# Optimization experiments

Hardware: AMD Instinct MI355X
Metric: run time of the kernel (lower is better)

## Reference

```python
import jax, jax.numpy as jnp
import numpy as np

C = 512        # num_channels
HEADS = 8      # num_channels // num_head_channels
DH = 64        # num_head_channels
G = 32         # num_groups
EPS = 1e-5
SCALE = DH ** -0.25  # pre-multiplied into q and k (scale applied twice -> 1/sqrt(DH))


def setup_inputs() -> dict:
    key = jax.random.key(0)
    ks = jax.random.split(key, 10)
    B, H, W = 2, 64, 64
    def w(k):
        return jax.random.normal(k, (C, C), jnp.float32) * 0.02
    def b(k):
        return jax.random.normal(k, (C,), jnp.float32) * 0.02
    return {
        "x": jax.random.normal(ks[0], (B, C, H, W), jnp.float32),
        "gn_w": jnp.ones((C,), jnp.float32),
        "gn_b": jnp.zeros((C,), jnp.float32),
        "wq": w(ks[1]), "bq": b(ks[2]),
        "wk": w(ks[3]), "bk": b(ks[4]),
        "wv": w(ks[5]), "bv": b(ks[6]),
        "wp": w(ks[7]), "bp": b(ks[8]),
    }


def reference(x, gn_w, gn_b, wq, bq, wk, bk, wv, bv, wp, bp):
    B, Cc, H, W = x.shape
    # GroupNorm over (C/G, H, W) per group
    xr = x.reshape(B, G, Cc // G, H * W)
    mean = xr.mean(axis=(2, 3), keepdims=True)
    var = xr.var(axis=(2, 3), keepdims=True)
    h = ((xr - mean) * jax.lax.rsqrt(var + EPS)).reshape(B, Cc, H, W)
    h = h * gn_w[None, :, None, None] + gn_b[None, :, None, None]
    # B C H W -> B (H W) C
    t = h.reshape(B, Cc, H * W).transpose(0, 2, 1)
    # q/k pre-multiplied by SCALE (equivalent to pre_multiply_weights_by_scale)
    q = (t @ wq.T + bq) * SCALE
    k = (t @ wk.T + bk) * SCALE
    v = t @ wv.T + bv
    def split_heads(a):  # B HW (h d) -> B h HW d
        return a.reshape(B, H * W, HEADS, DH).transpose(0, 2, 1, 3)
    q, k, v = split_heads(q), split_heads(k), split_heads(v)
    # full HWxHW score matrix, softmax over keys
    attn = jax.nn.softmax(jnp.einsum('bhqd,bhkd->bhqk', q, k), axis=-1)
    o = jnp.einsum('bhqk,bhkd->bhqd', attn, v)
    o = o.transpose(0, 2, 1, 3).reshape(B, H * W, Cc)  # join heads
    o = o @ wp.T + bp
    # B (H W) C -> B C H W, residual
    return o.transpose(0, 2, 1).reshape(B, Cc, H, W) + x
```

## Files before the change

kernel.cpp:

```cpp
#include <hip/hip_runtime.h>

#define HWN 4096
#define CCH 512
#define NHEAD 8
#define DHD 64
#define NBATCH 2
#define QK_SCALE 0.35355339059327373f
#define LOG2E    1.4426950408889634f

using floatx4 = __attribute__((ext_vector_type(4))) float;
using bf16x8  = __attribute__((ext_vector_type(8))) short;
using bf16x4  = __attribute__((ext_vector_type(4))) short;

__device__ __forceinline__ unsigned short f2b(float f) {
  union { float f; unsigned u; } x; x.f = f;
  unsigned r = x.u + 0x7FFFu + ((x.u >> 16) & 1u);
  return (unsigned short)(r >> 16);
}

__device__ __forceinline__ float fast_exp2(float x) {
#if __has_builtin(__builtin_amdgcn_exp2f)
  return __builtin_amdgcn_exp2f(x);
#else
  return __expf(x * 0.69314718056f);
#endif
}

__device__ __forceinline__ unsigned pack_bf16_trunc(float lo, float hi) {
  return __builtin_amdgcn_perm(__float_as_uint(hi), __float_as_uint(lo), 0x07060302u);
}

__global__ __launch_bounds__(256) void gn_stats(const float* __restrict__ x,
                                                float* __restrict__ stat) {
  int bg = blockIdx.x;
  const float4* p = (const float4*)(x + (size_t)bg * 65536) + blockIdx.y * 2048;
  float s = 0.f, ss = 0.f;
  for (int i = threadIdx.x; i < 2048; i += 256) {
    float4 v = p[i];
    s  += v.x + v.y + v.z + v.w;
    ss += v.x*v.x + v.y*v.y + v.z*v.z + v.w*v.w;
  }
  for (int off = 32; off; off >>= 1) {
    s  += __shfl_xor(s, off);
    ss += __shfl_xor(ss, off);
  }
  __shared__ float red[8];
  int w = threadIdx.x >> 6;
  if ((threadIdx.x & 63) == 0) { red[w] = s; red[4 + w] = ss; }
  __syncthreads();
  if (threadIdx.x == 0) {
    float S  = red[0] + red[1] + red[2] + red[3];
    float SS = red[4] + red[5] + red[6] + red[7];
    atomicAdd(&stat[bg], S);
    atomicAdd(&stat[64 + bg], SS);
  }
}

__global__ __launch_bounds__(256) void prep_w(
    const float* __restrict__ wq, const float* __restrict__ wk,
    const float* __restrict__ wv, const float* __restrict__ wp,
    const float* __restrict__ bq, const float* __restrict__ bk,
    const float* __restrict__ bv,
    unsigned short* __restrict__ Wqkv, unsigned short* __restrict__ Wp,
    float* __restrict__ bqkv) {
  int i = blockIdx.x * 256 + threadIdx.x;
  if (i < 786432) {
    int row = i >> 9;
    float v;
    if (row < 512)       v = wq[i] * (QK_SCALE * LOG2E);
    else if (row < 1024) v = wk[i - 262144] * QK_SCALE;
    else                 v = wv[i - 524288];
    Wqkv[i] = f2b(v);
  } else if (i < 1048576) {
    Wp[i - 786432] = f2b(wp[i - 786432]);
  } else if (i < 1050112) {
    int j = i - 1048576;
    float v = (j < 512) ? bq[j] * (QK_SCALE * LOG2E)
            : (j < 1024) ? bk[j - 512] * QK_SCALE
            : bv[j - 1024];
    bqkv[j] = v;
  }
}

__global__ __launch_bounds__(256) void gn_apply(
    const float* __restrict__ x, const float* __restrict__ stat,
    const float* __restrict__ gnw, const float* __restrict__ gnb,
    unsigned short* __restrict__ t) {
  int pt = blockIdx.x & 63;
  int ct = (blockIdx.x >> 6) & 7;
  int b  = blockIdx.x >> 9;
  int c0 = ct * 64, p0 = pt * 64;
  __shared__ float tile[64][68];
  int tid = threadIdx.x;
  for (int pp = 0; pp < 4; ++pp) {
    int f = (pp * 256 + tid) * 4;
    int cl = f >> 6, pl = f & 63;
    int c = c0 + cl;
    float4 v = *(const float4*)(x + ((size_t)(b * 512 + c)) * 4096 + p0 + pl);
    int g = c >> 4;
    float S    = stat[b * 32 + g];
    float SS   = stat[64 + b * 32 + g];
    float mean = S * (1.f / 65536.f);
    float var  = SS * (1.f / 65536.f) - mean * mean;
    float rstd = rsqrtf(var + 1e-5f);
    float w  = gnw[c] * rstd;
    float bb = gnb[c] - mean * w;
    tile[cl][pl + 0] = v.x * w + bb;
    tile[cl][pl + 1] = v.y * w + bb;
    tile[cl][pl + 2] = v.z * w + bb;
    tile[cl][pl + 3] = v.w * w + bb;
  }
  __syncthreads();
  for (int pp = 0; pp < 2; ++pp) {
    int f = (pp * 256 + tid) * 8;
    int pl = f >> 6, cl = f & 63;
    unsigned short u[8];
#pragma unroll
    for (int j = 0; j < 8; ++j) u[j] = f2b(tile[cl + j][pl]);
    *(uint4*)(t + ((size_t)(b * 4096 + p0 + pl)) * 512 + c0 + cl) = *(uint4*)u;
  }
}

__global__ __launch_bounds__(256) void gemm_qkv(
    const unsigned short* __restrict__ t, const unsigned short* __restrict__ Wqkv,
    const float* __restrict__ bqkv,
    unsigned short* __restrict__ qo, unsigned short* __restrict__ ko,
    unsigned short* __restrict__ vo) {
  int M0 = blockIdx.x * 64;
  int N0 = blockIdx.y * 64;
  __shared__ unsigned short At[64][72];
  __shared__ unsigned short Bt[64][72];
  int tid = threadIdx.x, w = tid >> 6, l = tid & 63;
  int quad = l >> 4, m16 = l & 15;
  floatx4 acc[4] = {};
  for (int k0 = 0; k0 < 512; k0 += 64) {
    __syncthreads();
#pragma unroll
    for (int pp = 0; pp < 2; ++pp) {
      int f = (pp * 256 + tid) * 8;
      int r = f >> 6, c = f & 63;
      *(uint4*)&At[r][c] = *(const uint4*)(t    + (size_t)(M0 + r) * 512 + k0 + c);
      *(uint4*)&Bt[r][c] = *(const uint4*)(Wqkv + (size_t)(N0 + r) * 512 + k0 + c);
    }
    __syncthreads();
    bf16x8 af0 = *(const bf16x8*)&At[w * 16 + m16][quad * 8];
    bf16x8 af1 = *(const bf16x8*)&At[w * 16 + m16][32 + quad * 8];
#pragma unroll
    for (int nt = 0; nt < 4; ++nt) {
      bf16x8 b0 = *(const bf16x8*)&Bt[nt * 16 + m16][quad * 8];
      bf16x8 b1 = *(const bf16x8*)&Bt[nt * 16 + m16][32 + quad * 8];
      acc[nt] = __builtin_amdgcn_mfma_f32_16x16x32_bf16(af0, b0, acc[nt], 0, 0, 0);
      acc[nt] = __builtin_amdgcn_mfma_f32_16x16x32_bf16(af1, b1, acc[nt], 0, 0, 0);
    }
  }
  int which = N0 >> 9;
  int head  = (N0 & 511) >> 6;
  if (which == 2) {
    __syncthreads();
#pragma unroll
    for (int nt = 0; nt < 4; ++nt) {
      int d = nt * 16 + m16;
      float bias = bqkv[N0 + d];
#pragma unroll
      for (int r = 0; r < 4; ++r)
        At[d][w * 16 + quad * 4 + r] = f2b(acc[nt][r] + bias);
    }
    __syncthreads();
    int bb = M0 >> 12, p0 = M0 & 4095;
    unsigned short* dst = vo + ((size_t)(bb * 8 + head) * 64) * 4096;
#pragma unroll
    for (int pp = 0; pp < 2; ++pp) {
      int f = (pp * 256 + tid) * 8;
      int d = f >> 6, pl = f & 63;
      *(uint4*)(dst + (size_t)d * 4096 + p0 + pl) = *(uint4*)&At[d][pl];
    }
  } else {
    unsigned short* dst = (which == 0) ? qo : ko;
#pragma unroll
    for (int nt = 0; nt < 4; ++nt) {
      int n = N0 + nt * 16 + m16;
      float bias = bqkv[n];
      int d = n & 63;
#pragma unroll
      for (int r = 0; r < 4; ++r) {
        int m = M0 + w * 16 + quad * 4 + r;
        int b = m >> 12, p = m & 4095;
        dst[(((size_t)(b * 8 + head) * 4096 + p) << 6) + d] = f2b(acc[nt][r] + bias);
      }
    }
  }
}

__global__ __launch_bounds__(256, 2) void attn(
    const unsigned short* __restrict__ q, const unsigned short* __restrict__ k,
    const unsigned short* __restrict__ vt, unsigned short* __restrict__ o) {
  int qt = blockIdx.x;
  int bh = blockIdx.y;
  int b = bh >> 3, h = bh & 7;
  __shared__ unsigned short Kt[128][72];
  __shared__ unsigned short Vt[64][136];
  int tid = threadIdx.x, w = tid >> 6, l = tid & 63;
  int quad = l >> 4, m16 = l & 15;
  const size_t base = (size_t)bh * HWN * DHD;
  int krow_base = ((m16 >> 2) * 8) + (m16 & 3);

  bf16x8 qfA0, qfA1, qfB0, qfB1;
  {
    int qrow = qt * 128 + w * 32 + m16;
    const unsigned short* qp = q + base + (size_t)qrow * 64 + quad * 8;
    qfA0 = *(const bf16x8*)qp;
    qfA1 = *(const bf16x8*)(qp + 32);
    qfB0 = *(const bf16x8*)(qp + 16 * 64);
    qfB1 = *(const bf16x8*)(qp + 16 * 64 + 32);
  }
  bf16x8 ones;
#pragma unroll
  for (int z = 0; z < 8; ++z) ones[z] = (short)0x3F80;

  floatx4 accOA[4] = {}, accOB[4] = {};
  floatx4 accLA = {}, accLB = {};
  float mrowA = -1e30f, mrowB = -1e30f;

  for (int kt = 0; kt < 32; ++kt) {
    __syncthreads();
#pragma unroll
    for (int pp = 0; pp < 4; ++pp) {
      int f = (pp * 256 + tid) * 8;
      int rk = f >> 6, ck = f & 63;
      *(uint4*)&Kt[rk][ck] = *(const uint4*)(k + base + (size_t)(kt * 128 + rk) * 64 + ck);
      int rv = f >> 7, cv = f & 127;
      *(uint4*)&Vt[rv][cv] = *(const uint4*)(vt + base + (size_t)rv * 4096 + kt * 128 + cv);
    }
    __syncthreads();
    floatx4 sA[8], sB[8];
#pragma unroll
    for (int nt = 0; nt < 4; ++nt)
#pragma unroll
      for (int hh = 0; hh < 2; ++hh) {
        int row = nt * 32 + hh * 4 + krow_base;
        bf16x8 kf0 = *(const bf16x8*)&Kt[row][quad * 8];
        bf16x8 kf1 = *(const bf16x8*)&Kt[row][32 + quad * 8];
        floatx4 zA = {}, zB = {};
        zA = __builtin_amdgcn_mfma_f32_16x16x32_bf16(kf0, qfA0, zA, 0, 0, 0);
        sA[nt * 2 + hh] = __builtin_amdgcn_mfma_f32_16x16x32_bf16(kf1, qfA1, zA, 0, 0, 0);
        zB = __builtin_amdgcn_mfma_f32_16x16x32_bf16(kf0, qfB0, zB, 0, 0, 0);
        sB[nt * 2 + hh] = __builtin_amdgcn_mfma_f32_16x16x32_bf16(kf1, qfB1, zB, 0, 0, 0);
      }
    float mxA = sA[0][0], mxB = sB[0][0];
#pragma unroll
    for (int nt = 0; nt < 8; ++nt)
#pragma unroll
      for (int i = 0; i < 4; ++i) {
        mxA = fmaxf(mxA, sA[nt][i]);
        mxB = fmaxf(mxB, sB[nt][i]);
      }
    mxA = fmaxf(mxA, __shfl_xor(mxA, 16));
    mxA = fmaxf(mxA, __shfl_xor(mxA, 32));
    mxB = fmaxf(mxB, __shfl_xor(mxB, 16));
    mxB = fmaxf(mxB, __shfl_xor(mxB, 32));
    bool grew = (mxA > mrowA) || (mxB > mrowB);
    float mnA = fmaxf(mrowA, mxA);
    float mnB = fmaxf(mrowB, mxB);
#pragma unroll
    for (int nt = 0; nt < 8; ++nt)
#pragma unroll
      for (int i = 0; i < 4; ++i) {
        sA[nt][i] = fast_exp2(sA[nt][i] - mnA);
        sB[nt][i] = fast_exp2(sB[nt][i] - mnB);
      }
    if (__ballot(grew)) {
      float aA = fast_exp2(mrowA - mnA);
      float aB = fast_exp2(mrowB - mnB);
      float a0 = __shfl(aA, quad * 4 + 0), b0 = __shfl(aB, quad * 4 + 0);
      float a1 = __shfl(aA, quad * 4 + 1), b1 = __shfl(aB, quad * 4 + 1);
      float a2 = __shfl(aA, quad * 4 + 2), b2 = __shfl(aB, quad * 4 + 2);
      float a3 = __shfl(aA, quad * 4 + 3), b3 = __shfl(aB, quad * 4 + 3);
#pragma unroll
      for (int dt = 0; dt < 4; ++dt) {
        accOA[dt][0] *= a0; accOA[dt][1] *= a1; accOA[dt][2] *= a2; accOA[dt][3] *= a3;
        accOB[dt][0] *= b0; accOB[dt][1] *= b1; accOB[dt][2] *= b2; accOB[dt][3] *= b3;
      }
      accLA[0] *= a0; accLA[1] *= a1; accLA[2] *= a2; accLA[3] *= a3;
      accLB[0] *= b0; accLB[1] *= b1; accLB[2] *= b2; accLB[3] *= b3;
    }
    mrowA = mnA; mrowB = mnB;
    bf16x8 pfA[4], pfB[4];
#pragma unroll
    for (int nt = 0; nt < 4; ++nt) {
      union { unsigned u[4]; bf16x8 v; } pa, pb;
      pa.u[0] = pack_bf16_trunc(sA[nt * 2][0],     sA[nt * 2][1]);
      pa.u[1] = pack_bf16_trunc(sA[nt * 2][2],     sA[nt * 2][3]);
      pa.u[2] = pack_bf16_trunc(sA[nt * 2 + 1][0], sA[nt * 2 + 1][1]);
      pa.u[3] = pack_bf16_trunc(sA[nt * 2 + 1][2], sA[nt * 2 + 1][3]);
      pfA[nt] = pa.v;
      pb.u[0] = pack_bf16_trunc(sB[nt * 2][0],     sB[nt * 2][1]);
      pb.u[1] = pack_bf16_trunc(sB[nt * 2][2],     sB[nt * 2][3]);
      pb.u[2] = pack_bf16_trunc(sB[nt * 2 + 1][0], sB[nt * 2 + 1][1]);
      pb.u[3] = pack_bf16_trunc(sB[nt * 2 + 1][2], sB[nt * 2 + 1][3]);
      pfB[nt] = pb.v;
    }
#pragma unroll
    for (int dt = 0; dt < 4; ++dt) {
#pragma unroll
      for (int nt = 0; nt < 4; ++nt) {
        bf16x8 vf = *(const bf16x8*)&Vt[dt * 16 + m16][nt * 32 + quad * 8];
        accOA[dt] = __builtin_amdgcn_mfma_f32_16x16x32_bf16(pfA[nt], vf, accOA[dt], 0, 0, 0);
        accOB[dt] = __builtin_amdgcn_mfma_f32_16x16x32_bf16(pfB[nt], vf, accOB[dt], 0, 0, 0);
      }
    }
#pragma unroll
    for (int nt = 0; nt < 4; ++nt) {
      accLA = __builtin_amdgcn_mfma_f32_16x16x32_bf16(pfA[nt], ones, accLA, 0, 0, 0);
      accLB = __builtin_amdgcn_mfma_f32_16x16x32_bf16(pfB[nt], ones, accLB, 0, 0, 0);
    }
  }
  float lA0 = 1.f / accLA[0], lA1 = 1.f / accLA[1], lA2 = 1.f / accLA[2], lA3 = 1.f / accLA[3];
  float lB0 = 1.f / accLB[0], lB1 = 1.f / accLB[1], lB2 = 1.f / accLB[2], lB3 = 1.f / accLB[3];
#pragma unroll
  for (int dt = 0; dt < 4; ++dt) {
    int d = dt * 16 + m16;
    int qrowA = qt * 128 + w * 32 + quad * 4;
    size_t rowb = ((size_t)(b * 4096 + qrowA)) * 512 + h * 64 + d;
    o[rowb]           = f2b(accOA[dt][0] * lA0);
    o[rowb + 512]     = f2b(accOA[dt][1] * lA1);
    o[rowb + 1024]    = f2b(accOA[dt][2] * lA2);
    o[rowb + 1536]    = f2b(accOA[dt][3] * lA3);
    size_t rowb2 = rowb + (size_t)16 * 512;
    o[rowb2]          = f2b(accOB[dt][0] * lB0);
    o[rowb2 + 512]    = f2b(accOB[dt][1] * lB1);
    o[rowb2 + 1024]   = f2b(accOB[dt][2] * lB2);
    o[rowb2 + 1536]   = f2b(accOB[dt][3] * lB3);
  }
}

__global__ __launch_bounds__(256) void gemm_out(
    const unsigned short* __restrict__ o, const unsigned short* __restrict__ Wp,
    const float* __restrict__ bp, const float* __restrict__ x,
    float* __restrict__ out) {
  int C0 = blockIdx.x * 64, P0 = blockIdx.y * 64, b = blockIdx.z;
  __shared__ unsigned short At[64][72];
  __shared__ unsigned short Bt[64][72];
  int tid = threadIdx.x, w = tid >> 6, l = tid & 63;
  int quad = l >> 4, m16 = l & 15;
  floatx4 acc[4] = {};
  for (int k0 = 0; k0 < 512; k0 += 64) {
    __syncthreads();
#pragma unroll
    for (int pp = 0; pp < 2; ++pp) {
      int f = (pp * 256 + tid) * 8;
      int r = f >> 6, c = f & 63;
      *(uint4*)&At[r][c] = *(const uint4*)(Wp + (size_t)(C0 + r) * 512 + k0 + c);
      *(uint4*)&Bt[r][c] = *(const uint4*)(o + ((size_t)(b * 4096 + P0 + r)) * 512 + k0 + c);
    }
    __syncthreads();
    bf16x8 af0 = *(const bf16x8*)&At[w * 16 + m16][quad * 8];
    bf16x8 af1 = *(const bf16x8*)&At[w * 16 + m16][32 + quad * 8];
#pragma unroll
    for (int nt = 0; nt < 4; ++nt) {
      bf16x8 b0 = *(const bf16x8*)&Bt[nt * 16 + m16][quad * 8];
      bf16x8 b1 = *(const bf16x8*)&Bt[nt * 16 + m16][32 + quad * 8];
      acc[nt] = __builtin_amdgcn_mfma_f32_16x16x32_bf16(af0, b0, acc[nt], 0, 0, 0);
      acc[nt] = __builtin_amdgcn_mfma_f32_16x16x32_bf16(af1, b1, acc[nt], 0, 0, 0);
    }
  }
#pragma unroll
  for (int r = 0; r < 4; ++r) {
    int c = C0 + w * 16 + quad * 4 + r;
    float bias = bp[c];
#pragma unroll
    for (int nt = 0; nt < 4; ++nt) {
      int p = P0 + nt * 16 + m16;
      size_t idx = ((size_t)(b * 512 + c)) * 4096 + p;
      out[idx] = acc[nt][r] + bias + x[idx];
    }
  }
}

extern "C" void kernel_launch(void* const* d_in, const int* in_sizes, int n_in,
                              void* d_out, int out_size, void* d_ws, size_t ws_size,
                              hipStream_t stream) {
  const float* x   = (const float*)d_in[0];
  const float* gnw = (const float*)d_in[1];
  const float* gnb = (const float*)d_in[2];
  const float* wq  = (const float*)d_in[3];
  const float* bq  = (const float*)d_in[4];
  const float* wk  = (const float*)d_in[5];
  const float* bk  = (const float*)d_in[6];
  const float* wv  = (const float*)d_in[7];
  const float* bv  = (const float*)d_in[8];
  const float* wp  = (const float*)d_in[9];
  const float* bp  = (const float*)d_in[10];
  float* out = (float*)d_out;

  char* ws = (char*)d_ws;
  float* stat          = (float*)ws;          ws += 1024;
  float* bqkv          = (float*)ws;          ws += 8192;
  unsigned short* Wqkv = (unsigned short*)ws; ws += (size_t)1536 * 512 * 2;
  unsigned short* Wp   = (unsigned short*)ws; ws += (size_t)512 * 512 * 2;
  unsigned short* t    = (unsigned short*)ws; ws += (size_t)8192 * 512 * 2;
  unsigned short* qb   = (unsigned short*)ws; ws += (size_t)8192 * 512 * 2;
  unsigned short* kb   = (unsigned short*)ws; ws += (size_t)8192 * 512 * 2;
  unsigned short* vb   = (unsigned short*)ws; ws += (size_t)8192 * 512 * 2;
  unsigned short* ob   = (unsigned short*)ws; ws += (size_t)8192 * 512 * 2;

  hipMemsetAsync(stat, 0, 512, stream);
  dim3 g0(64, 8);
  gn_stats<<<g0, 256, 0, stream>>>(x, stat);
  prep_w<<<4103, 256, 0, stream>>>(wq, wk, wv, wp, bq, bk, bv, Wqkv, Wp, bqkv);
  gn_apply<<<1024, 256, 0, stream>>>(x, stat, gnw, gnb, t);
  dim3 g1(128, 24);
  gemm_qkv<<<g1, 256, 0, stream>>>(t, Wqkv, bqkv, qb, kb, vb);
  dim3 g2(32, 16);
  attn<<<g2, 256, 0, stream>>>(qb, kb, vb, ob);
  dim3 g3(8, 64, 2);
  gemm_out<<<g3, 256, 0, stream>>>(ob, Wp, bp, x, out);
}
```

Before: 276.2 us.

## Split attention over two key halves and merge partial softmax results

The attention kernel now splits the key range into two halves along a new grid dimension, doubling the block count from 512 to 1024. It also raises the launch-bounds occupancy hint from 2 to 4 blocks. Each block writes a normalized partial output plus its row max and sum, reusing the output buffer and the t buffer as scratch. A new merge kernel rescales and combines the two partials into the final bf16 head output. This targets under-filled CUs (512 blocks on a 256-CU GPU) at the cost of an extra kernel launch, extra memory traffic, and an additional bf16 rounding of the partial outputs.

```diff
diff --git a/kernel.cpp b/kernel.cpp
--- a/kernel.cpp
+++ b/kernel.cpp
@@ -16,6 +16,11 @@
   union { float f; unsigned u; } x; x.f = f;
   unsigned r = x.u + 0x7FFFu + ((x.u >> 16) & 1u);
   return (unsigned short)(r >> 16);
+}
+
+__device__ __forceinline__ float b2f(unsigned short u) {
+  union { unsigned u; float f; } x; x.u = ((unsigned)u) << 16;
+  return x.f;
 }
 
 __device__ __forceinline__ float fast_exp2(float x) {
@@ -191,17 +196,19 @@
   }
 }
 
-__global__ __launch_bounds__(256, 2) void attn(
+__global__ __launch_bounds__(256, 4) void attn(
     const unsigned short* __restrict__ q, const unsigned short* __restrict__ k,
-    const unsigned short* __restrict__ vt, unsigned short* __restrict__ o) {
+    const unsigned short* __restrict__ vt,
+    unsigned short* __restrict__ pO, float* __restrict__ mlbuf) {
   int qt = blockIdx.x;
   int bh = blockIdx.y;
-  int b = bh >> 3, h = bh & 7;
+  int ks = blockIdx.z;
   __shared__ unsigned short Kt[128][72];
   __shared__ unsigned short Vt[64][136];
   int tid = threadIdx.x, w = tid >> 6, l = tid & 63;
   int quad = l >> 4, m16 = l & 15;
   const size_t base = (size_t)bh * HWN * DHD;
+  const int key0 = ks * 2048;
   int krow_base = ((m16 >> 2) * 8) + (m16 & 3);
 
   bf16x8 qfA0, qfA1, qfB0, qfB1;
@@ -221,15 +228,15 @@
   floatx4 accLA = {}, accLB = {};
   float mrowA = -1e30f, mrowB = -1e30f;
 
-  for (int kt = 0; kt < 32; ++kt) {
+  for (int kt = 0; kt < 16; ++kt) {
     __syncthreads();
 #pragma unroll
     for (int pp = 0; pp < 4; ++pp) {
       int f = (pp * 256 + tid) * 8;
       int rk = f >> 6, ck = f & 63;
-      *(uint4*)&Kt[rk][ck] = *(const uint4*)(k + base + (size_t)(kt * 128 + rk) * 64 + ck);
+      *(uint4*)&Kt[rk][ck] = *(const uint4*)(k + base + (size_t)(key0 + kt * 128 + rk) * 64 + ck);
       int rv = f >> 7, cv = f & 127;
-      *(uint4*)&Vt[rv][cv] = *(const uint4*)(vt + base + (size_t)rv * 4096 + kt * 128 + cv);
+      *(uint4*)&Vt[rv][cv] = *(const uint4*)(vt + base + (size_t)rv * 4096 + key0 + kt * 128 + cv);
     }
     __syncthreads();
     floatx4 sA[8], sB[8];
@@ -314,23 +321,70 @@
       accLB = __builtin_amdgcn_mfma_f32_16x16x32_bf16(pfB[nt], ones, accLB, 0, 0, 0);
     }
   }
+  const size_t prow = (size_t)(ks * 16 + bh) * 4096;
   float lA0 = 1.f / accLA[0], lA1 = 1.f / accLA[1], lA2 = 1.f / accLA[2], lA3 = 1.f / accLA[3];
   float lB0 = 1.f / accLB[0], lB1 = 1.f / accLB[1], lB2 = 1.f / accLB[2], lB3 = 1.f / accLB[3];
 #pragma unroll
   for (int dt = 0; dt < 4; ++dt) {
     int d = dt * 16 + m16;
     int qrowA = qt * 128 + w * 32 + quad * 4;
-    size_t rowb = ((size_t)(b * 4096 + qrowA)) * 512 + h * 64 + d;
-    o[rowb]           = f2b(accOA[dt][0] * lA0);
-    o[rowb + 512]     = f2b(accOA[dt][1] * lA1);
-    o[rowb + 1024]    = f2b(accOA[dt][2] * lA2);
-    o[rowb + 1536]    = f2b(accOA[dt][3] * lA3);
-    size_t rowb2 = rowb + (size_t)16 * 512;
-    o[rowb2]          = f2b(accOB[dt][0] * lB0);
-    o[rowb2 + 512]    = f2b(accOB[dt][1] * lB1);
-    o[rowb2 + 1024]   = f2b(accOB[dt][2] * lB2);
-    o[rowb2 + 1536]   = f2b(accOB[dt][3] * lB3);
-  }
+    size_t rb = (prow + qrowA) * 64 + d;
+    pO[rb]        = f2b(accOA[dt][0] * lA0);
+    pO[rb + 64]   = f2b(accOA[dt][1] * lA1);
+    pO[rb + 128]  = f2b(accOA[dt][2] * lA2);
+    pO[rb + 192]  = f2b(accOA[dt][3] * lA3);
+    size_t rb2 = rb + 16 * 64;
+    pO[rb2]       = f2b(accOB[dt][0] * lB0);
+    pO[rb2 + 64]  = f2b(accOB[dt][1] * lB1);
+    pO[rb2 + 128] = f2b(accOB[dt][2] * lB2);
+    pO[rb2 + 192] = f2b(accOB[dt][3] * lB3);
+  }
+  if (m16 < 4) {
+    float mvA = __shfl(mrowA, quad * 4 + m16);
+    float mvB = __shfl(mrowB, quad * 4 + m16);
+    float lvA = (m16 == 0) ? accLA[0] : (m16 == 1) ? accLA[1] : (m16 == 2) ? accLA[2] : accLA[3];
+    float lvB = (m16 == 0) ? accLB[0] : (m16 == 1) ? accLB[1] : (m16 == 2) ? accLB[2] : accLB[3];
+    int qrow = qt * 128 + w * 32 + quad * 4 + m16;
+    float2* mlp = (float2*)mlbuf;
+    float2 va; va.x = mvA; va.y = lvA;
+    float2 vb; vb.x = mvB; vb.y = lvB;
+    mlp[prow + qrow]      = va;
+    mlp[prow + qrow + 16] = vb;
+  }
+}
+
+__global__ __launch_bounds__(256) void attn_merge(
+    const unsigned short* __restrict__ pO, const float* __restrict__ mlbuf,
+    unsigned short* __restrict__ ob) {
+  int r = blockIdx.x * 64 + (threadIdx.x >> 2);
+  int dseg = (threadIdx.x & 3) * 16;
+  int bh = r >> 12, qq = r & 4095;
+  int b = bh >> 3, h = bh & 7;
+  const float2* mlp = (const float2*)mlbuf;
+  float2 ml0 = mlp[r];
+  float2 ml1 = mlp[65536 + r];
+  float ms = fmaxf(ml0.x, ml1.x);
+  float s0 = fast_exp2(ml0.x - ms) * ml0.y;
+  float s1 = fast_exp2(ml1.x - ms) * ml1.y;
+  float inv = 1.f / (s0 + s1);
+  float w0 = s0 * inv, w1 = s1 * inv;
+  const unsigned short* p0 = pO + ((size_t)r * 64 + dseg);
+  const unsigned short* p1 = p0 + (size_t)65536 * 64;
+  uint4 u0a = *(const uint4*)p0, u0b = *(const uint4*)(p0 + 8);
+  uint4 u1a = *(const uint4*)p1, u1b = *(const uint4*)(p1 + 8);
+  const unsigned short* a0 = (const unsigned short*)&u0a;
+  const unsigned short* a1 = (const unsigned short*)&u1a;
+  const unsigned short* b0p = (const unsigned short*)&u0b;
+  const unsigned short* b1p = (const unsigned short*)&u1b;
+  unsigned short u[16];
+#pragma unroll
+  for (int z = 0; z < 8; ++z) {
+    u[z]     = f2b(w0 * b2f(a0[z])  + w1 * b2f(a1[z]));
+    u[8 + z] = f2b(w0 * b2f(b0p[z]) + w1 * b2f(b1p[z]));
+  }
+  unsigned short* op = ob + ((size_t)(b * 4096 + qq)) * 512 + h * 64 + dseg;
+  *(uint4*)op       = *(uint4*)u;
+  *(uint4*)(op + 8) = *(uint4*)(u + 8);
 }
 
 __global__ __launch_bounds__(256) void gemm_out(
@@ -403,6 +457,9 @@
   unsigned short* vb   = (unsigned short*)ws; ws += (size_t)8192 * 512 * 2;
   unsigned short* ob   = (unsigned short*)ws; ws += (size_t)8192 * 512 * 2;
 
+  unsigned short* pO  = (unsigned short*)d_out;
+  float* mlbuf        = (float*)t;
+
   hipMemsetAsync(stat, 0, 512, stream);
   dim3 g0(64, 8);
   gn_stats<<<g0, 256, 0, stream>>>(x, stat);
@@ -410,8 +467,9 @@
   gn_apply<<<1024, 256, 0, stream>>>(x, stat, gnw, gnb, t);
   dim3 g1(128, 24);
   gemm_qkv<<<g1, 256, 0, stream>>>(t, Wqkv, bqkv, qb, kb, vb);
-  dim3 g2(32, 16);
-  attn<<<g2, 256, 0, stream>>>(qb, kb, vb, ob);
+  dim3 g2(32, 16, 2);
+  attn<<<g2, 256, 0, stream>>>(qb, kb, vb, pO, mlbuf);
+  attn_merge<<<1024, 256, 0, stream>>>(pO, mlbuf, ob);
   dim3 g3(8, 64, 2);
   gemm_out<<<g3, 256, 0, stream>>>(ob, Wp, bp, x, out);
 }
```

Result: slower. 389.7 us (+41.1%).
